# Kernel tuning notes

Measured on AMD Instinct MI355X. Metric: run time of the kernel, lower is better.

## Reference

```python
import jax, jax.numpy as jnp
import numpy as np

D_MODEL = 1024
N_HEADS = 16
HEAD_DIM = D_MODEL // N_HEADS


def setup_inputs() -> dict:
    key = jax.random.key(0)
    ks = jax.random.split(key, 9)
    s = 1.0 / np.sqrt(D_MODEL)
    x = jax.random.normal(ks[0], (2, 2048, D_MODEL), dtype=jnp.float32)
    Wq = jax.random.uniform(ks[1], (D_MODEL, D_MODEL), jnp.float32, -s, s)
    bq = jax.random.uniform(ks[2], (D_MODEL,), jnp.float32, -s, s)
    Wk = jax.random.uniform(ks[3], (D_MODEL, D_MODEL), jnp.float32, -s, s)
    bk = jax.random.uniform(ks[4], (D_MODEL,), jnp.float32, -s, s)
    Wv = jax.random.uniform(ks[5], (D_MODEL, D_MODEL), jnp.float32, -s, s)
    bv = jax.random.uniform(ks[6], (D_MODEL,), jnp.float32, -s, s)
    Wo = jax.random.uniform(ks[7], (D_MODEL, D_MODEL), jnp.float32, -s, s)
    bo = jax.random.uniform(ks[8], (D_MODEL,), jnp.float32, -s, s)
    return {"x": x, "Wq": Wq, "bq": bq, "Wk": Wk, "bk": bk,
            "Wv": Wv, "bv": bv, "Wo": Wo, "bo": bo}


def reference(x, Wq, bq, Wk, bk, Wv, bv, Wo, bo):
    B, L, _ = x.shape
    # Linear projections (torch Linear: y = x @ W.T + b; here W stored as [in, out])
    def split_heads(t):  # [B, L, D] -> [B, H, L, hd]
        return t.reshape(B, L, N_HEADS, HEAD_DIM).transpose(0, 2, 1, 3)
    Q = split_heads(x @ Wq + bq)
    K = split_heads(x @ Wk + bk)
    V = split_heads(x @ Wv + bv)
    scores = jnp.einsum('bhqd,bhkd->bhqk', Q, K) / np.sqrt(HEAD_DIM).astype(np.float32)
    attn = jax.nn.softmax(scores, axis=-1)
    out = jnp.einsum('bhqk,bhkd->bhqd', attn, V)
    out = out.transpose(0, 2, 1, 3).reshape(B, L, D_MODEL)
    return out @ Wo + bo
```

## Files before the change

### kernel.cpp

```cpp
#include <hip/hip_runtime.h>

typedef float f32x4  __attribute__((ext_vector_type(4)));
typedef short s16x8  __attribute__((ext_vector_type(8)));
typedef short s16x4  __attribute__((ext_vector_type(4)));
typedef unsigned short u16x8 __attribute__((ext_vector_type(8)));
typedef unsigned int   u32x2 __attribute__((ext_vector_type(2)));

#define DM   1024
#define LSEQ 2048
#define NH   16
#define HD   64
#define MTOT 4096
#define RS   3072
#define NT   (LSEQ / 64)

__device__ __forceinline__ unsigned short f2bf(float f) {
  union { float f; unsigned int u; } v; v.f = f;
  unsigned int r = (v.u + 0x7fffu + ((v.u >> 16) & 1u)) >> 16;
  return (unsigned short)r;
}

__device__ __forceinline__ unsigned cvtpk(float lo, float hi) {
  unsigned r;
  asm volatile("v_cvt_pk_bf16_f32 %0, %1, %2" : "=v"(r) : "v"(lo), "v"(hi));
  return r;
}

__global__ __launch_bounds__(256) void xconv(const float* __restrict__ x,
                                             unsigned short* __restrict__ xb) {
  long i = ((long)blockIdx.x * 256 + threadIdx.x) * 8;
  float4 a = *(const float4*)&x[i];
  float4 b = *(const float4*)&x[i + 4];
  u16x8 o;
  o[0] = f2bf(a.x); o[1] = f2bf(a.y); o[2] = f2bf(a.z); o[3] = f2bf(a.w);
  o[4] = f2bf(b.x); o[5] = f2bf(b.y); o[6] = f2bf(b.z); o[7] = f2bf(b.w);
  *(u16x8*)&xb[i] = o;
}

__global__ __launch_bounds__(256) void wtrans4(const float* __restrict__ W0,
                                               const float* __restrict__ W1,
                                               const float* __restrict__ W2,
                                               const float* __restrict__ W3,
                                               unsigned short* __restrict__ Wt) {
  __shared__ __align__(16) unsigned short t[64][72];
  const int z = blockIdx.z;
  const float* W = (z == 0) ? W0 : (z == 1) ? W1 : (z == 2) ? W2 : W3;
  unsigned short* dst = Wt + (size_t)z * DM * DM;
  const int n0 = blockIdx.x * 64, k0 = blockIdx.y * 64;
  const int r = threadIdx.x >> 4, c4 = (threadIdx.x & 15) * 4;
#pragma unroll
  for (int rr = r; rr < 64; rr += 16) {
    float4 v = *(const float4*)&W[(long)(k0 + rr) * DM + n0 + c4];
    ushort4 u;
    u.x = f2bf(v.x); u.y = f2bf(v.y); u.z = f2bf(v.z); u.w = f2bf(v.w);
    *(ushort4*)&t[rr][c4] = u;
  }
  __syncthreads();
#pragma unroll
  for (int rr = r; rr < 64; rr += 16) {
    ushort4 u;
    u.x = t[c4 + 0][rr]; u.y = t[c4 + 1][rr];
    u.z = t[c4 + 2][rr]; u.w = t[c4 + 3][rr];
    *(ushort4*)&dst[(long)(n0 + rr) * DM + k0 + c4] = u;
  }
}

__global__ __launch_bounds__(256) void vtrans(const unsigned short* __restrict__ QKV,
                                              unsigned short* __restrict__ VT) {
  __shared__ __align__(16) unsigned short t[64][72];
  const int bh = blockIdx.y, st = blockIdx.x;
  const int b = bh >> 4, h = bh & 15;
  const int r = threadIdx.x >> 3, c8 = (threadIdx.x & 7) * 8;
#pragma unroll
  for (int rr = r; rr < 64; rr += 32) {
    const unsigned short* Vg = QKV + (size_t)(b * LSEQ + st * 64 + rr) * RS + 2 * DM + h * HD;
    *(u16x8*)&t[rr][c8] = *(const u16x8*)&Vg[c8];
  }
  __syncthreads();
  unsigned short* Vo = VT + (size_t)(bh * HD) * LSEQ + st * 64;
#pragma unroll
  for (int rr = r; rr < 64; rr += 32) {
    u16x8 u;
#pragma unroll
    for (int j = 0; j < 8; ++j) u[j] = t[c8 + j][rr];
    *(u16x8*)&Vo[(size_t)rr * LSEQ + c8] = u;
  }
}

template <int QKV_MODE>
__global__ __launch_bounds__(256) void gemm_bt(
    const unsigned short* __restrict__ A, const unsigned short* __restrict__ Bt,
    const float* __restrict__ bias0, const float* __restrict__ bias1,
    const float* __restrict__ bias2, void* __restrict__ Cout, int N, int K) {
  __shared__ __align__(16) unsigned short As[128][72];
  __shared__ __align__(16) unsigned short Bs[128][72];
  const int tid = threadIdx.x;
  const int lane = tid & 63, w = tid >> 6;
  const int r16 = lane & 15, g = lane >> 4;
  const int m0 = blockIdx.y * 128, n0 = blockIdx.x * 128;
  const int wm = (w >> 1) * 64, wn = (w & 1) * 64;
  const int srow = tid >> 2, scol = (tid & 3) * 8;
  f32x4 acc[4][4] = {};
  for (int kt = 0; kt < K; kt += 64) {
    const unsigned short* Ag = A + (long)(m0 + srow) * K + kt + scol;
    const unsigned short* Bg = Bt + (long)(n0 + srow) * K + kt + scol;
    s16x8 a0 = *(const s16x8*)Ag;
    s16x8 a1 = *(const s16x8*)(Ag + 32);
    s16x8 a2 = *(const s16x8*)(Ag + 64L * K);
    s16x8 a3 = *(const s16x8*)(Ag + 64L * K + 32);
    s16x8 b0 = *(const s16x8*)Bg;
    s16x8 b1 = *(const s16x8*)(Bg + 32);
    s16x8 b2 = *(const s16x8*)(Bg + 64L * K);
    s16x8 b3 = *(const s16x8*)(Bg + 64L * K + 32);
    __syncthreads();
    *(s16x8*)&As[srow][scol]           = a0;
    *(s16x8*)&As[srow][scol + 32]      = a1;
    *(s16x8*)&As[srow + 64][scol]      = a2;
    *(s16x8*)&As[srow + 64][scol + 32] = a3;
    *(s16x8*)&Bs[srow][scol]           = b0;
    *(s16x8*)&Bs[srow][scol + 32]      = b1;
    *(s16x8*)&Bs[srow + 64][scol]      = b2;
    *(s16x8*)&Bs[srow + 64][scol + 32] = b3;
    __syncthreads();
#pragma unroll
    for (int kk = 0; kk < 64; kk += 32) {
      s16x8 af[4], bf[4];
#pragma unroll
      for (int i = 0; i < 4; i++) af[i] = *(const s16x8*)&As[wm + i * 16 + r16][kk + g * 8];
#pragma unroll
      for (int j = 0; j < 4; j++) bf[j] = *(const s16x8*)&Bs[wn + j * 16 + r16][kk + g * 8];
#pragma unroll
      for (int i = 0; i < 4; i++)
#pragma unroll
        for (int j = 0; j < 4; j++)
          acc[i][j] = __builtin_amdgcn_mfma_f32_16x16x32_bf16(af[i], bf[j], acc[i][j], 0, 0, 0);
    }
  }
#pragma unroll
  for (int i = 0; i < 4; i++) {
#pragma unroll
    for (int j = 0; j < 4; j++) {
      const int row = m0 + wm + i * 16 + g * 4;
      const int col = n0 + wn + j * 16 + r16;
      float bb, sc = 1.0f;
      if constexpr (QKV_MODE) {
        bb = (col < 1024) ? bias0[col] : (col < 2048) ? bias1[col - 1024] : bias2[col - 2048];
        if (col < 1024) sc = 0.18033688011112042f;
      } else {
        bb = bias0[col];
      }
#pragma unroll
      for (int r = 0; r < 4; r++) {
        float v = (acc[i][j][r] + bb) * sc;
        if constexpr (QKV_MODE)
          ((unsigned short*)Cout)[(long)(row + r) * N + col] = f2bf(v);
        else
          ((float*)Cout)[(long)(row + r) * N + col] = v;
      }
    }
  }
}

__global__ __launch_bounds__(256) void attn7(const unsigned short* __restrict__ QKV,
                                             const unsigned short* __restrict__ VT,
                                             unsigned short* __restrict__ O) {
  __shared__ __align__(16) unsigned short Ks[2][64][76];
  __shared__ __align__(16) unsigned short Vs[2][64][76];
  __shared__ float Lsum[4][16];
  const int tid = threadIdx.x;
  const int lane = tid & 63, w = tid >> 6;
  const int r16 = lane & 15, g = lane >> 4;
  const int qb = blockIdx.x, bh = blockIdx.y;
  const int b = bh >> 4, h = bh & 15;

  const unsigned short* Qg = QKV + (size_t)(b * LSEQ + qb * 64 + w * 16 + r16) * RS + h * HD;
  const s16x8 qa0 = *(const s16x8*)&Qg[g * 8];
  const s16x8 qa1 = *(const s16x8*)&Qg[32 + g * 8];

  const unsigned short* Kb = QKV + (size_t)(b * LSEQ) * RS + DM + h * HD;
  const unsigned short* Vb = VT + (size_t)(bh * HD) * LSEQ;
  const int srow = tid >> 2, scol = (tid & 3) * 8;

  f32x4 o[4] = {};
  float psum[4] = {0.f, 0.f, 0.f, 0.f};

  s16x8 k0 = *(const s16x8*)&Kb[(size_t)srow * RS + scol];
  s16x8 k1 = *(const s16x8*)&Kb[(size_t)srow * RS + scol + 32];
  s16x8 v0 = *(const s16x8*)&Vb[(size_t)srow * LSEQ + scol];
  s16x8 v1 = *(const s16x8*)&Vb[(size_t)srow * LSEQ + scol + 32];
  *(s16x8*)&Ks[0][srow][scol]      = k0;
  *(s16x8*)&Ks[0][srow][scol + 32] = k1;
  *(s16x8*)&Vs[0][srow][scol]      = v0;
  *(s16x8*)&Vs[0][srow][scol + 32] = v1;
  __syncthreads();

  for (int t = 0; t < NT; ++t) {
    const int cur = t & 1;
    if (t + 1 < NT) {
      const size_t ko = (size_t)((t + 1) * 64 + srow) * RS + scol;
      const size_t vo = (size_t)srow * LSEQ + (t + 1) * 64 + scol;
      k0 = *(const s16x8*)&Kb[ko];
      k1 = *(const s16x8*)&Kb[ko + 32];
      v0 = *(const s16x8*)&Vb[vo];
      v1 = *(const s16x8*)&Vb[vo + 32];
    }

    f32x4 s[4];
#pragma unroll
    for (int kc = 0; kc < 4; kc++) {
      s16x8 kb0 = *(const s16x8*)&Ks[cur][kc * 16 + r16][g * 8];
      s16x8 kb1 = *(const s16x8*)&Ks[cur][kc * 16 + r16][32 + g * 8];
      f32x4 z = {};
      z = __builtin_amdgcn_mfma_f32_16x16x32_bf16(kb0, qa0, z, 0, 0, 0);
      s[kc] = __builtin_amdgcn_mfma_f32_16x16x32_bf16(kb1, qa1, z, 0, 0, 0);
    }

    s16x4 pa[4];
#pragma unroll
    for (int kc = 0; kc < 4; kc++) {
      float p0 = exp2f(s[kc][0]);
      float p1 = exp2f(s[kc][1]);
      float p2 = exp2f(s[kc][2]);
      float p3 = exp2f(s[kc][3]);
      psum[0] += p0; psum[1] += p1; psum[2] += p2; psum[3] += p3;
      u32x2 pk = {cvtpk(p0, p1), cvtpk(p2, p3)};
      pa[kc] = __builtin_bit_cast(s16x4, pk);
    }

#pragma unroll
    for (int kc = 0; kc < 4; kc++)
#pragma unroll
      for (int dc = 0; dc < 4; dc++) {
        s16x4 vb = *(const s16x4*)&Vs[cur][dc * 16 + r16][kc * 16 + 4 * g];
        o[dc] = __builtin_amdgcn_mfma_f32_16x16x16bf16_1k(pa[kc], vb, o[dc], 0, 0, 0);
      }

    if (t + 1 < NT) {
      *(s16x8*)&Ks[cur ^ 1][srow][scol]      = k0;
      *(s16x8*)&Ks[cur ^ 1][srow][scol + 32] = k1;
      *(s16x8*)&Vs[cur ^ 1][srow][scol]      = v0;
      *(s16x8*)&Vs[cur ^ 1][srow][scol + 32] = v1;
      __syncthreads();
    }
  }

  float tot = psum[0] + psum[1] + psum[2] + psum[3];
  tot += __shfl_xor(tot, 16);
  tot += __shfl_xor(tot, 32);
  if (g == 0) Lsum[w][r16] = tot;
  __syncthreads();
  const float4 sv = *(const float4*)&Lsum[w][4 * g];

  unsigned short* Og = O + (size_t)(b * LSEQ + qb * 64 + w * 16) * DM + h * HD;
#pragma unroll
  for (int r = 0; r < 4; r++) {
    const float inv = 1.0f / ((const float*)&sv)[r];
#pragma unroll
    for (int dc = 0; dc < 4; dc++)
      Og[(size_t)(g * 4 + r) * DM + dc * 16 + r16] = f2bf(o[dc][r] * inv);
  }
}

extern "C" void kernel_launch(void* const* d_in, const int* in_sizes, int n_in,
                              void* d_out, int out_size, void* d_ws, size_t ws_size,
                              hipStream_t stream) {
  const float* x  = (const float*)d_in[0];
  const float* Wq = (const float*)d_in[1];
  const float* bq = (const float*)d_in[2];
  const float* Wk = (const float*)d_in[3];
  const float* bk = (const float*)d_in[4];
  const float* Wv = (const float*)d_in[5];
  const float* bv = (const float*)d_in[6];
  const float* Wo = (const float*)d_in[7];
  const float* bo = (const float*)d_in[8];

  unsigned short* xb   = (unsigned short*)d_ws;
  unsigned short* Wcat = xb + (size_t)MTOT * DM;
  unsigned short* Wot  = Wcat + (size_t)3 * DM * DM;
  unsigned short* QKVb = Wot + (size_t)DM * DM;
  unsigned short* Ob   = QKVb + (size_t)MTOT * 3 * DM;
  unsigned short* VTb  = xb;

  xconv<<<(MTOT * DM) / (256 * 8), 256, 0, stream>>>(x, xb);
  wtrans4<<<dim3(16, 16, 4), 256, 0, stream>>>(Wq, Wk, Wv, Wo, Wcat);

  gemm_bt<1><<<dim3(3 * DM / 128, MTOT / 128), 256, 0, stream>>>(
      xb, Wcat, bq, bk, bv, (void*)QKVb, 3 * DM, DM);
  vtrans<<<dim3(LSEQ / 64, 2 * NH), 256, 0, stream>>>(QKVb, VTb);
  attn7<<<dim3(LSEQ / 64, 2 * NH), 256, 0, stream>>>(QKVb, VTb, Ob);
  gemm_bt<0><<<dim3(DM / 128, MTOT / 128), 256, 0, stream>>>(
      Ob, Wot, bo, nullptr, nullptr, d_out, DM, DM);
}
```

Measured before the change: 156.0 us.

## Double query rows per attention block and prefetch next GEMM tile into registers

The attention kernel now has each wave process 32 query rows instead of 16, so every K/V tile loaded into shared memory is reused by twice as many queries. The grid is halved to match, which cuts K/V global traffic and barrier count per query. The GEMM now issues the global loads for the next K-tile right after the shared-memory store, so they overlap with the MFMA work on the current tile. The costs are higher register pressure in both kernels and half as many attention blocks, which may lower occupancy and how well the work spreads across CUs.

```diff
diff --git a/kernel.cpp b/kernel.cpp
--- a/kernel.cpp
+++ b/kernel.cpp
@@ -100,18 +100,18 @@
   const int m0 = blockIdx.y * 128, n0 = blockIdx.x * 128;
   const int wm = (w >> 1) * 64, wn = (w & 1) * 64;
   const int srow = tid >> 2, scol = (tid & 3) * 8;
+  const unsigned short* Ag = A + (long)(m0 + srow) * K + scol;
+  const unsigned short* Bg = Bt + (long)(n0 + srow) * K + scol;
   f32x4 acc[4][4] = {};
+  s16x8 a0 = *(const s16x8*)Ag;
+  s16x8 a1 = *(const s16x8*)(Ag + 32);
+  s16x8 a2 = *(const s16x8*)(Ag + 64L * K);
+  s16x8 a3 = *(const s16x8*)(Ag + 64L * K + 32);
+  s16x8 b0 = *(const s16x8*)Bg;
+  s16x8 b1 = *(const s16x8*)(Bg + 32);
+  s16x8 b2 = *(const s16x8*)(Bg + 64L * K);
+  s16x8 b3 = *(const s16x8*)(Bg + 64L * K + 32);
   for (int kt = 0; kt < K; kt += 64) {
-    const unsigned short* Ag = A + (long)(m0 + srow) * K + kt + scol;
-    const unsigned short* Bg = Bt + (long)(n0 + srow) * K + kt + scol;
-    s16x8 a0 = *(const s16x8*)Ag;
-    s16x8 a1 = *(const s16x8*)(Ag + 32);
-    s16x8 a2 = *(const s16x8*)(Ag + 64L * K);
-    s16x8 a3 = *(const s16x8*)(Ag + 64L * K + 32);
-    s16x8 b0 = *(const s16x8*)Bg;
-    s16x8 b1 = *(const s16x8*)(Bg + 32);
-    s16x8 b2 = *(const s16x8*)(Bg + 64L * K);
-    s16x8 b3 = *(const s16x8*)(Bg + 64L * K + 32);
     __syncthreads();
     *(s16x8*)&As[srow][scol]           = a0;
     *(s16x8*)&As[srow][scol + 32]      = a1;
@@ -122,6 +122,18 @@
     *(s16x8*)&Bs[srow + 64][scol]      = b2;
     *(s16x8*)&Bs[srow + 64][scol + 32] = b3;
     __syncthreads();
+    if (kt + 64 < K) {
+      const unsigned short* An = Ag + kt + 64;
+      const unsigned short* Bn = Bg + kt + 64;
+      a0 = *(const s16x8*)An;
+      a1 = *(const s16x8*)(An + 32);
+      a2 = *(const s16x8*)(An + 64L * K);
+      a3 = *(const s16x8*)(An + 64L * K + 32);
+      b0 = *(const s16x8*)Bn;
+      b1 = *(const s16x8*)(Bn + 32);
+      b2 = *(const s16x8*)(Bn + 64L * K);
+      b3 = *(const s16x8*)(Bn + 64L * K + 32);
+    }
 #pragma unroll
     for (int kk = 0; kk < 64; kk += 32) {
       s16x8 af[4], bf[4];
@@ -161,28 +173,33 @@
   }
 }
 
-__global__ __launch_bounds__(256) void attn7(const unsigned short* __restrict__ QKV,
+__global__ __launch_bounds__(256) void attn8(const unsigned short* __restrict__ QKV,
                                              const unsigned short* __restrict__ VT,
                                              unsigned short* __restrict__ O) {
   __shared__ __align__(16) unsigned short Ks[2][64][76];
   __shared__ __align__(16) unsigned short Vs[2][64][76];
-  __shared__ float Lsum[4][16];
+  __shared__ float Lsum[4][32];
   const int tid = threadIdx.x;
   const int lane = tid & 63, w = tid >> 6;
   const int r16 = lane & 15, g = lane >> 4;
   const int qb = blockIdx.x, bh = blockIdx.y;
   const int b = bh >> 4, h = bh & 15;
 
-  const unsigned short* Qg = QKV + (size_t)(b * LSEQ + qb * 64 + w * 16 + r16) * RS + h * HD;
-  const s16x8 qa0 = *(const s16x8*)&Qg[g * 8];
-  const s16x8 qa1 = *(const s16x8*)&Qg[32 + g * 8];
+  const unsigned short* QgA =
+      QKV + (size_t)(b * LSEQ + qb * 128 + w * 32 + r16) * RS + h * HD;
+  const unsigned short* QgB = QgA + 16 * RS;
+  const s16x8 qa0 = *(const s16x8*)&QgA[g * 8];
+  const s16x8 qa1 = *(const s16x8*)&QgA[32 + g * 8];
+  const s16x8 qb0 = *(const s16x8*)&QgB[g * 8];
+  const s16x8 qb1 = *(const s16x8*)&QgB[32 + g * 8];
 
   const unsigned short* Kb = QKV + (size_t)(b * LSEQ) * RS + DM + h * HD;
   const unsigned short* Vb = VT + (size_t)(bh * HD) * LSEQ;
   const int srow = tid >> 2, scol = (tid & 3) * 8;
 
-  f32x4 o[4] = {};
-  float psum[4] = {0.f, 0.f, 0.f, 0.f};
+  f32x4 oA[4] = {}, oB[4] = {};
+  float psA[4] = {0.f, 0.f, 0.f, 0.f};
+  float psB[4] = {0.f, 0.f, 0.f, 0.f};
 
   s16x8 k0 = *(const s16x8*)&Kb[(size_t)srow * RS + scol];
   s16x8 k1 = *(const s16x8*)&Kb[(size_t)srow * RS + scol + 32];
@@ -205,26 +222,35 @@
       v1 = *(const s16x8*)&Vb[vo + 32];
     }
 
-    f32x4 s[4];
+    f32x4 sA[4], sB[4];
 #pragma unroll
     for (int kc = 0; kc < 4; kc++) {
       s16x8 kb0 = *(const s16x8*)&Ks[cur][kc * 16 + r16][g * 8];
       s16x8 kb1 = *(const s16x8*)&Ks[cur][kc * 16 + r16][32 + g * 8];
-      f32x4 z = {};
-      z = __builtin_amdgcn_mfma_f32_16x16x32_bf16(kb0, qa0, z, 0, 0, 0);
-      s[kc] = __builtin_amdgcn_mfma_f32_16x16x32_bf16(kb1, qa1, z, 0, 0, 0);
-    }
-
-    s16x4 pa[4];
+      f32x4 zA = {}, zB = {};
+      zA = __builtin_amdgcn_mfma_f32_16x16x32_bf16(kb0, qa0, zA, 0, 0, 0);
+      sA[kc] = __builtin_amdgcn_mfma_f32_16x16x32_bf16(kb1, qa1, zA, 0, 0, 0);
+      zB = __builtin_amdgcn_mfma_f32_16x16x32_bf16(kb0, qb0, zB, 0, 0, 0);
+      sB[kc] = __builtin_amdgcn_mfma_f32_16x16x32_bf16(kb1, qb1, zB, 0, 0, 0);
+    }
+
+    s16x4 paA[4], paB[4];
 #pragma unroll
     for (int kc = 0; kc < 4; kc++) {
-      float p0 = exp2f(s[kc][0]);
-      float p1 = exp2f(s[kc][1]);
-      float p2 = exp2f(s[kc][2]);
-      float p3 = exp2f(s[kc][3]);
-      psum[0] += p0; psum[1] += p1; psum[2] += p2; psum[3] += p3;
-      u32x2 pk = {cvtpk(p0, p1), cvtpk(p2, p3)};
-      pa[kc] = __builtin_bit_cast(s16x4, pk);
+      float a0f = exp2f(sA[kc][0]);
+      float a1f = exp2f(sA[kc][1]);
+      float a2f = exp2f(sA[kc][2]);
+      float a3f = exp2f(sA[kc][3]);
+      psA[0] += a0f; psA[1] += a1f; psA[2] += a2f; psA[3] += a3f;
+      u32x2 pkA = {cvtpk(a0f, a1f), cvtpk(a2f, a3f)};
+      paA[kc] = __builtin_bit_cast(s16x4, pkA);
+      float b0f = exp2f(sB[kc][0]);
+      float b1f = exp2f(sB[kc][1]);
+      float b2f = exp2f(sB[kc][2]);
+      float b3f = exp2f(sB[kc][3]);
+      psB[0] += b0f; psB[1] += b1f; psB[2] += b2f; psB[3] += b3f;
+      u32x2 pkB = {cvtpk(b0f, b1f), cvtpk(b2f, b3f)};
+      paB[kc] = __builtin_bit_cast(s16x4, pkB);
     }
 
 #pragma unroll
@@ -232,7 +258,8 @@
 #pragma unroll
       for (int dc = 0; dc < 4; dc++) {
         s16x4 vb = *(const s16x4*)&Vs[cur][dc * 16 + r16][kc * 16 + 4 * g];
-        o[dc] = __builtin_amdgcn_mfma_f32_16x16x16bf16_1k(pa[kc], vb, o[dc], 0, 0, 0);
+        oA[dc] = __builtin_amdgcn_mfma_f32_16x16x16bf16_1k(paA[kc], vb, oA[dc], 0, 0, 0);
+        oB[dc] = __builtin_amdgcn_mfma_f32_16x16x16bf16_1k(paB[kc], vb, oB[dc], 0, 0, 0);
       }
 
     if (t + 1 < NT) {
@@ -244,20 +271,30 @@
     }
   }
 
-  float tot = psum[0] + psum[1] + psum[2] + psum[3];
-  tot += __shfl_xor(tot, 16);
-  tot += __shfl_xor(tot, 32);
-  if (g == 0) Lsum[w][r16] = tot;
+  float totA = psA[0] + psA[1] + psA[2] + psA[3];
+  totA += __shfl_xor(totA, 16);
+  totA += __shfl_xor(totA, 32);
+  float totB = psB[0] + psB[1] + psB[2] + psB[3];
+  totB += __shfl_xor(totB, 16);
+  totB += __shfl_xor(totB, 32);
+  if (g == 0) {
+    Lsum[w][r16]      = totA;
+    Lsum[w][16 + r16] = totB;
+  }
   __syncthreads();
-  const float4 sv = *(const float4*)&Lsum[w][4 * g];
-
-  unsigned short* Og = O + (size_t)(b * LSEQ + qb * 64 + w * 16) * DM + h * HD;
+  const float4 svA = *(const float4*)&Lsum[w][4 * g];
+  const float4 svB = *(const float4*)&Lsum[w][16 + 4 * g];
+
+  unsigned short* Og = O + (size_t)(b * LSEQ + qb * 128 + w * 32) * DM + h * HD;
 #pragma unroll
   for (int r = 0; r < 4; r++) {
-    const float inv = 1.0f / ((const float*)&sv)[r];
-#pragma unroll
-    for (int dc = 0; dc < 4; dc++)
-      Og[(size_t)(g * 4 + r) * DM + dc * 16 + r16] = f2bf(o[dc][r] * inv);
+    const float invA = 1.0f / ((const float*)&svA)[r];
+    const float invB = 1.0f / ((const float*)&svB)[r];
+#pragma unroll
+    for (int dc = 0; dc < 4; dc++) {
+      Og[(size_t)(g * 4 + r) * DM + dc * 16 + r16]        = f2bf(oA[dc][r] * invA);
+      Og[(size_t)(16 + g * 4 + r) * DM + dc * 16 + r16]   = f2bf(oB[dc][r] * invB);
+    }
   }
 }
 
@@ -287,7 +324,7 @@
   gemm_bt<1><<<dim3(3 * DM / 128, MTOT / 128), 256, 0, stream>>>(
       xb, Wcat, bq, bk, bv, (void*)QKVb, 3 * DM, DM);
   vtrans<<<dim3(LSEQ / 64, 2 * NH), 256, 0, stream>>>(QKVb, VTb);
-  attn7<<<dim3(LSEQ / 64, 2 * NH), 256, 0, stream>>>(QKVb, VTb, Ob);
+  attn8<<<dim3(LSEQ / 128, 2 * NH), 256, 0, stream>>>(QKVb, VTb, Ob);
   gemm_bt<0><<<dim3(DM / 128, MTOT / 128), 256, 0, stream>>>(
       Ob, Wot, bo, nullptr, nullptr, d_out, DM, DM);
 }
```

Measured after the change: 146.6 us. 6.1% less time.
